# Kernel optimization log

Hardware: AMD Instinct MI355X
Metric: run time of the kernel (lower is better)

## Reference

```python
import jax, jax.numpy as jnp
import numpy as np

N, E, H, OUT, L = 50000, 500000, 256, 128, 2
EPS = 1e-5  # torch LayerNorm default


def _make_edges(k):
    # both rows cover all N nodes so that unique()/remap in the original is identity
    k1, k2, kp = jax.random.split(k, 3)
    row0 = jnp.concatenate([jax.random.permutation(kp, N), jax.random.randint(k1, (E - N,), 0, N)])
    row1 = jnp.concatenate([jnp.arange(N), jax.random.randint(k2, (E - N,), 0, N)])
    return jnp.stack([row0, row1]).astype(jnp.int32)


def setup_inputs() -> dict:
    key = jax.random.key(0)
    ks = jax.random.split(key, 7)
    s = 0.02
    x = jax.random.normal(ks[0], (N, H), jnp.float32)
    edge_r1 = _make_edges(ks[1])
    edge_r2 = _make_edges(ks[2])
    Wl = jax.random.normal(ks[3], (L, H, H), jnp.float32) * s
    W0 = jax.random.normal(ks[4], (L, H, H), jnp.float32) * s
    W1 = jax.random.normal(ks[5], (L, H, H), jnp.float32) * s
    bl = jnp.zeros((L, H), jnp.float32)
    b0 = jnp.zeros((L, H), jnp.float32)
    b1 = jnp.zeros((L, H), jnp.float32)
    gamma = jnp.ones((L, H), jnp.float32)
    beta = jnp.zeros((L, H), jnp.float32)
    Wout = jax.random.normal(ks[6], (OUT, H), jnp.float32) * s
    bout = jnp.zeros((OUT,), jnp.float32)
    return dict(x=x, edge_r1=edge_r1, edge_r2=edge_r2, Wl=Wl, bl=bl, W0=W0, b0=b0,
                W1=W1, b1=b1, gamma=gamma, beta=beta, Wout=Wout, bout=bout)


def _layer(i, h, x0, e, Wl, bl, W0, b0, W1, b1, gamma, beta):
    # PyG flow='target_to_source', aggr='add': gather h at e[1], scatter-add at e[0]
    agg = jax.ops.segment_sum(h[e[1]], e[0], num_segments=h.shape[0])  # [N, H]
    z = agg @ Wl[i].T + bl[i] + h @ W0[i].T + b0[i] + x0 @ W1[i].T + b1[i]
    z = jax.nn.relu(z)
    mu = jnp.mean(z, axis=-1, keepdims=True)
    var = jnp.mean(jnp.square(z - mu), axis=-1, keepdims=True)
    return (z - mu) * jax.lax.rsqrt(var + EPS) * gamma[i] + beta[i]  # dropout is identity in eval


def reference(x, edge_r1, edge_r2, Wl, bl, W0, b0, W1, b1, gamma, beta, Wout, bout):
    # reversed(metapath): (C,r2,C) with conv_idx=1 first, then (C,r1,C) with conv_idx=0
    h = _layer(1, x, x, edge_r2, Wl, bl, W0, b0, W1, b1, gamma, beta)
    h = _layer(0, h, x, edge_r1, Wl, bl, W0, b0, W1, b1, gamma, beta)
    return h @ Wout.T + bout  # [N, OUT]
```

## Files before the change

kernel.cpp:

```cpp
#include <hip/hip_runtime.h>
#include <stdint.h>

#define N_NODES 50000
#define N_EDGES 500000
#define NPAD    50048
#define NSCAN   196
#define EPS     1e-5f

typedef _Float16 half8_ __attribute__((ext_vector_type(8)));
typedef _Float16 half4_ __attribute__((ext_vector_type(4)));
typedef float    float4_ __attribute__((ext_vector_type(4)));

typedef uint32_t u32_g __attribute__((address_space(1)));
typedef uint32_t u32_s __attribute__((address_space(3)));

__device__ __forceinline__ void gload16(const void* g, void* lds_wave_base) {
    __builtin_amdgcn_global_load_lds((const u32_g*)g, (u32_s*)lds_wave_base, 16, 0, 0);
}

__global__ __launch_bounds__(256) void prep_kernel(
        const int* __restrict__ e1, const int* __restrict__ e2,
        int* __restrict__ cnt, int* __restrict__ ranks,
        const float* __restrict__ x, _Float16* __restrict__ xh,
        _Float16* __restrict__ aggb, _Float16* __restrict__ h1,
        const float* __restrict__ Wl, const float* __restrict__ W0,
        const float* __restrict__ W1, const float* __restrict__ Wout,
        _Float16* __restrict__ Wcat,
        const float* __restrict__ bl, const float* __restrict__ b0,
        const float* __restrict__ b1, const float* __restrict__ bout,
        float* __restrict__ bias) {
    const int bid = blockIdx.x;
    const int tid = threadIdx.x;
    if (bid < 490) {
        const int set = (bid >= 245);
        const int bx  = set ? bid - 245 : bid;
        const int* dst = set ? e2 : e1;
        int* c = cnt + set * N_NODES;
        int* r = ranks + set * N_EDGES;
        int i0 = (bx * 256 + tid) * 8;
        if (i0 >= N_EDGES) return;
        int4 d0 = *(const int4*)(dst + i0);
        int4 d1 = *(const int4*)(dst + i0 + 4);
        int r0 = atomicAdd(&c[d0.x], 1);
        int r1 = atomicAdd(&c[d0.y], 1);
        int r2 = atomicAdd(&c[d0.z], 1);
        int r3 = atomicAdd(&c[d0.w], 1);
        int r4 = atomicAdd(&c[d1.x], 1);
        int r5 = atomicAdd(&c[d1.y], 1);
        int r6 = atomicAdd(&c[d1.z], 1);
        int r7 = atomicAdd(&c[d1.w], 1);
        *(int4*)(r + i0)     = make_int4(r0, r1, r2, r3);
        *(int4*)(r + i0 + 4) = make_int4(r4, r5, r6, r7);
    } else if (bid < 12990) {
        int i = (bid - 490) * 256 + tid;
        float4_ v = ((const float4_*)x)[i];
        half4_ h;
        h[0] = (_Float16)v[0]; h[1] = (_Float16)v[1];
        h[2] = (_Float16)v[2]; h[3] = (_Float16)v[3];
        ((half4_*)xh)[i] = h;
    } else if (bid < 14654) {
        int i = (bid - 12990) * 256 + tid;
        if (i < 2 * 256 * 768) {
            int l = i / (256 * 768);
            int r = i % (256 * 768);
            int j = r / 768, k = r % 768;
            const float* s = (k < 256) ? Wl : (k < 512 ? W0 : W1);
            Wcat[i] = (_Float16)s[l * 65536 + j * 256 + (k & 255)];
        } else {
            Wcat[i] = (_Float16)Wout[i - 2 * 256 * 768];
        }
    } else if (bid < 14690) {
        int j = (bid - 14654) * 256 + tid;
        int buf = j / 3072, jj = j % 3072;
        _Float16* p = (buf == 0) ? xh : (buf == 1) ? aggb : h1;
        half4_ z = {(_Float16)0.f, (_Float16)0.f, (_Float16)0.f, (_Float16)0.f};
        *(half4_*)(p + (size_t)N_NODES * 256 + (size_t)jj * 4) = z;
    } else {
        int i = (bid - 14690) * 256 + tid;
        if (i < 512)      bias[i] = bl[i] + b0[i] + b1[i];
        else if (i < 640) bias[i] = bout[i - 512];
    }
}

__global__ __launch_bounds__(256) void scan_kernel(const int* __restrict__ cnt,
                                                   unsigned long long* __restrict__ state,
                                                   int* __restrict__ rp) {
    __shared__ int sm[256];
    __shared__ int s_excl;
    const int bid = blockIdx.x;
    const int set = bid / NSCAN;
    const int seq = bid % NSCAN;
    const int t = threadIdx.x;
    const int i = seq * 256 + t;
    const int* c = cnt + set * N_NODES;
    int* rpS = rp + set * (N_NODES + 1);
    unsigned long long* st = state + set * NSCAN;

    int v = (i < N_NODES) ? c[i] : 0;
    sm[t] = v;
    __syncthreads();
    for (int off = 1; off < 256; off <<= 1) {
        int x = sm[t];
        if (t >= off) x += sm[t - off];
        __syncthreads();
        sm[t] = x;
        __syncthreads();
    }
    int total = sm[255];

    if (t == 0) {
        if (seq == 0) {
            atomicExch(&st[0], (2ULL << 32) | (unsigned int)total);
            s_excl = 0;
        } else {
            atomicExch(&st[seq], (1ULL << 32) | (unsigned int)total);
            int running = 0;
            int j = seq - 1;
            while (true) {
                unsigned long long s = atomicAdd(&st[j], 0ULL);
                unsigned int tag = (unsigned int)(s >> 32);
                if (tag == 0) continue;
                running += (int)(unsigned int)s;
                if (tag == 2) break;
                j--;
            }
            atomicExch(&st[seq], (2ULL << 32) | (unsigned int)(running + total));
            s_excl = running;
        }
    }
    __syncthreads();
    int excl = s_excl;
    if (i < N_NODES) rpS[i] = sm[t] - v + excl;
    if (seq == NSCAN - 1 && t == 0) rpS[N_NODES] = excl + total;
}

__global__ void place_kernel(const int* __restrict__ e1, const int* __restrict__ e2,
                             const int* __restrict__ ranks, const int* __restrict__ rp,
                             int* __restrict__ col, int e, int n) {
    const int set = blockIdx.y;
    const int* ed = set ? e2 : e1;
    const int* r  = ranks + set * e;
    const int* rpS = rp + set * (n + 1);
    int* cl = col + set * e;
    int i0 = (blockIdx.x * 256 + threadIdx.x) * 8;
    if (i0 >= e) return;
    int4 d0 = *(const int4*)(ed + i0);
    int4 d1 = *(const int4*)(ed + i0 + 4);
    int4 s0 = *(const int4*)(ed + e + i0);
    int4 s1 = *(const int4*)(ed + e + i0 + 4);
    int4 k0 = *(const int4*)(r + i0);
    int4 k1 = *(const int4*)(r + i0 + 4);
    int p0 = rpS[d0.x] + k0.x;
    int p1 = rpS[d0.y] + k0.y;
    int p2 = rpS[d0.z] + k0.z;
    int p3 = rpS[d0.w] + k0.w;
    int p4 = rpS[d1.x] + k1.x;
    int p5 = rpS[d1.y] + k1.y;
    int p6 = rpS[d1.z] + k1.z;
    int p7 = rpS[d1.w] + k1.w;
    cl[p0] = s0.x; cl[p1] = s0.y; cl[p2] = s0.z; cl[p3] = s0.w;
    cl[p4] = s1.x; cl[p5] = s1.y; cl[p6] = s1.z; cl[p7] = s1.w;
}

__global__ void gather_kernel(const _Float16* __restrict__ hin,
                              const int* __restrict__ rowptr, const int* __restrict__ col,
                              _Float16* __restrict__ dst, int n) {
    int node = blockIdx.x * 4 + (threadIdx.x >> 6);
    int lane = threadIdx.x & 63;
    int half = lane >> 5, l5 = lane & 31;
    if (node >= n) return;
    int s = rowptr[node], e = rowptr[node + 1];
    float a[8] = {0.f, 0.f, 0.f, 0.f, 0.f, 0.f, 0.f, 0.f};
    float b[8] = {0.f, 0.f, 0.f, 0.f, 0.f, 0.f, 0.f, 0.f};
    int i = s + half;
    for (; i + 2 < e; i += 4) {
        int c0 = col[i], c1 = col[i + 2];
        half8_ v0 = *(const half8_*)(hin + (size_t)c0 * 256 + l5 * 8);
        half8_ v1 = *(const half8_*)(hin + (size_t)c1 * 256 + l5 * 8);
#pragma unroll
        for (int j = 0; j < 8; j++) { a[j] += (float)v0[j]; b[j] += (float)v1[j]; }
    }
    for (; i < e; i += 2) {
        int c0 = col[i];
        half8_ v0 = *(const half8_*)(hin + (size_t)c0 * 256 + l5 * 8);
#pragma unroll
        for (int j = 0; j < 8; j++) a[j] += (float)v0[j];
    }
    half8_ o;
#pragma unroll
    for (int j = 0; j < 8; j++) {
        float t = a[j] + b[j];
        t += __shfl_xor(t, 32, 64);
        o[j] = (_Float16)t;
    }
    if (half == 0)
        *(half8_*)(dst + (size_t)node * 256 + l5 * 8) = o;
}

template <bool OUTFUSE>
__global__ __launch_bounds__(512) void gemm_ln(const _Float16* __restrict__ agg,
                                               const _Float16* __restrict__ hsrc,
                                               const _Float16* __restrict__ xh,
                                               const _Float16* __restrict__ Bw,
                                               const float* __restrict__ bias,
                                               const float* __restrict__ gamma,
                                               const float* __restrict__ beta,
                                               _Float16* __restrict__ H,
                                               const _Float16* __restrict__ WoutH,
                                               const float* __restrict__ biasOut,
                                               float* __restrict__ Out) {
    __shared__ __align__(16) char smem[49152];
    char* AsB = smem;
    char* BsB = smem + 16384;
    const int rowBase = blockIdx.x * 128;
    const int tid  = threadIdx.x;
    const int lane = tid & 63;
    const int w    = tid >> 6;
    const int wm = w & 1, wn = w >> 1;
    const int quad = lane >> 4, mr = lane & 15;
    const int x7 = mr & 7;

    float4_ acc[4][4];
#pragma unroll
    for (int i = 0; i < 4; i++)
#pragma unroll
        for (int j = 0; j < 4; j++) { float4_ z4 = {0.f, 0.f, 0.f, 0.f}; acc[i][j] = z4; }

    int cA0 = w * 64 + lane, cA1 = cA0 + 512;
    int rA0 = cA0 >> 3, rA1 = cA1 >> 3;
    size_t offA0 = (size_t)(rowBase + rA0) * 256 + (((cA0 & 7) ^ (rA0 & 7)) * 8);
    size_t offA1 = (size_t)(rowBase + rA1) * 256 + (((cA1 & 7) ^ (rA1 & 7)) * 8);
    size_t offB[4];
#pragma unroll
    for (int j = 0; j < 4; j++) {
        int c = j * 512 + w * 64 + lane;
        int r = c >> 3;
        offB[j] = (size_t)r * 768 + (((c & 7) ^ (r & 7)) * 8);
    }
    void* lA0 = AsB + w * 1024;
    void* lA1 = AsB + 8192 + w * 1024;

    for (int k0 = 0; k0 < 768; k0 += 64) {
        const _Float16* src = (k0 < 256) ? agg : (k0 < 512) ? hsrc : xh;
        const int kloc = k0 & 255;
        gload16(src + offA0 + kloc, lA0);
        gload16(src + offA1 + kloc, lA1);
        gload16(Bw + offB[0] + k0, BsB + w * 1024);
        gload16(Bw + offB[1] + k0, BsB + 8192 + w * 1024);
        gload16(Bw + offB[2] + k0, BsB + 16384 + w * 1024);
        gload16(Bw + offB[3] + k0, BsB + 24576 + w * 1024);
        __syncthreads();
#pragma unroll
        for (int s = 0; s < 2; s++) {
            half8_ a[4], b[4];
#pragma unroll
            for (int im = 0; im < 4; im++) {
                int row = wm * 64 + im * 16 + mr;
                a[im] = *(const half8_*)(AsB + row * 128 + (((s * 4 + quad) ^ x7) * 16));
            }
#pragma unroll
            for (int in = 0; in < 4; in++) {
                int row = wn * 64 + in * 16 + mr;
                b[in] = *(const half8_*)(BsB + row * 128 + (((s * 4 + quad) ^ x7) * 16));
            }
#pragma unroll
            for (int im = 0; im < 4; im++)
#pragma unroll
                for (int in = 0; in < 4; in++)
                    acc[im][in] = __builtin_amdgcn_mfma_f32_16x16x32_f16(a[im], b[in], acc[im][in], 0, 0, 0);
        }
        __syncthreads();
    }

    float bv[4], gv[4], bev[4];
#pragma unroll
    for (int in = 0; in < 4; in++) {
        int colg = wn * 64 + in * 16 + mr;
        bv[in]  = bias[colg];
        gv[in]  = gamma[colg];
        bev[in] = beta[colg];
    }
    float* lnbuf   = (float*)AsB;
    float* lnstats = (float*)(AsB + 4096);

#pragma unroll
    for (int im = 0; im < 4; im++)
#pragma unroll
        for (int r = 0; r < 4; r++) {
            float s = 0.f, sq = 0.f;
#pragma unroll
            for (int in = 0; in < 4; in++) {
                float v = acc[im][in][r] + bv[in];
                v = v > 0.f ? v : 0.f;
                s += v; sq += v * v;
            }
            s  += __shfl_xor(s, 1, 64);  sq += __shfl_xor(sq, 1, 64);
            s  += __shfl_xor(s, 2, 64);  sq += __shfl_xor(sq, 2, 64);
            s  += __shfl_xor(s, 4, 64);  sq += __shfl_xor(sq, 4, 64);
            s  += __shfl_xor(s, 8, 64);  sq += __shfl_xor(sq, 8, 64);
            if (mr == 0) {
                int rl = wm * 64 + im * 16 + quad * 4 + r;
                lnbuf[(wn * 128 + rl) * 2]     = s;
                lnbuf[(wn * 128 + rl) * 2 + 1] = sq;
            }
        }
    __syncthreads();
    if (tid < 128) {
        float s  = lnbuf[tid * 2]             + lnbuf[(128 + tid) * 2]
                 + lnbuf[(256 + tid) * 2]     + lnbuf[(384 + tid) * 2];
        float sq = lnbuf[tid * 2 + 1]         + lnbuf[(128 + tid) * 2 + 1]
                 + lnbuf[(256 + tid) * 2 + 1] + lnbuf[(384 + tid) * 2 + 1];
        float mu  = s * (1.0f / 256.0f);
        float var = sq * (1.0f / 256.0f) - mu * mu;
        lnstats[tid * 2]     = mu;
        lnstats[tid * 2 + 1] = rsqrtf(var + EPS);
    }
    __syncthreads();

    float bvo[4];
    if (OUTFUSE) {
#pragma unroll
        for (int ct = 0; ct < 4; ct++)
            bvo[ct] = biasOut[(w >> 2) * 64 + ct * 16 + mr];
    }

    _Float16* BsH = (_Float16*)BsB;
#pragma unroll
    for (int p = 0; p < 2; p++) {
        if (wm == p) {
#pragma unroll
            for (int im = 0; im < 4; im++)
#pragma unroll
                for (int r = 0; r < 4; r++) {
                    int rl = im * 16 + quad * 4 + r;
                    float mu = lnstats[(p * 64 + rl) * 2];
                    float rs = lnstats[(p * 64 + rl) * 2 + 1];
#pragma unroll
                    for (int in = 0; in < 4; in++) {
                        float v = acc[im][in][r] + bv[in];
                        v = v > 0.f ? v : 0.f;
                        int colg = wn * 64 + in * 16 + mr;
                        int off2 = rl * 256 + (((colg >> 3) ^ (rl & 31)) << 3) + (colg & 7);
                        BsH[off2] = (_Float16)((v - mu) * rs * gv[in] + bev[in]);
                    }
                }
        }
        __syncthreads();
        if (!OUTFUSE) {
#pragma unroll
            for (int i = 0; i < 4; i++) {
                int c = i * 512 + tid;
                int row = c >> 5, ch = c & 31;
                half8_ v = *(const half8_*)(BsB + row * 512 + ((ch ^ (row & 31)) << 4));
                *(half8_*)(H + (size_t)(rowBase + p * 64 + row) * 256 + ch * 8) = v;
            }
        } else {
            const int rt = w & 3;
            const int chh = w >> 2;
            float4_ acc2[4];
#pragma unroll
            for (int ct = 0; ct < 4; ct++) { float4_ z4 = {0.f, 0.f, 0.f, 0.f}; acc2[ct] = z4; }
            const int rA = rt * 16 + mr;
#pragma unroll
            for (int s2 = 0; s2 < 8; s2++) {
                int ck = s2 * 4 + quad;
                half8_ a2 = *(const half8_*)(BsB + rA * 512 + ((ck ^ (rA & 31)) << 4));
#pragma unroll
                for (int ct = 0; ct < 4; ct++) {
                    int colg = chh * 64 + ct * 16 + mr;
                    half8_ b2 = *(const half8_*)(WoutH + (size_t)colg * 256 + s2 * 32 + quad * 8);
                    acc2[ct] = __builtin_amdgcn_mfma_f32_16x16x32_f16(a2, b2, acc2[ct], 0, 0, 0);
                }
            }
#pragma unroll
            for (int ct = 0; ct < 4; ct++) {
                int colg = chh * 64 + ct * 16 + mr;
#pragma unroll
                for (int r = 0; r < 4; r++) {
                    int row = rowBase + p * 64 + rt * 16 + quad * 4 + r;
                    if (row < N_NODES)
                        Out[(size_t)row * 128 + colg] = acc2[ct][r] + bvo[ct];
                }
            }
        }
        __syncthreads();
    }
}

extern "C" void kernel_launch(void* const* d_in, const int* in_sizes, int n_in,
                              void* d_out, int out_size, void* d_ws, size_t ws_size,
                              hipStream_t stream) {
    const float* x    = (const float*)d_in[0];
    const int*   e1   = (const int*)d_in[1];
    const int*   e2   = (const int*)d_in[2];
    const float* Wl   = (const float*)d_in[3];
    const float* bl   = (const float*)d_in[4];
    const float* W0   = (const float*)d_in[5];
    const float* b0   = (const float*)d_in[6];
    const float* W1   = (const float*)d_in[7];
    const float* b1   = (const float*)d_in[8];
    const float* gamma= (const float*)d_in[9];
    const float* beta = (const float*)d_in[10];
    const float* Wout = (const float*)d_in[11];
    const float* bout = (const float*)d_in[12];

    char* ws = (char*)d_ws;
    size_t off = 0;
    auto alloc = [&](size_t bytes) -> char* {
        char* p = ws + off;
        off = (off + bytes + 255) & ~(size_t)255;
        return p;
    };
    _Float16* xh   = (_Float16*)alloc((size_t)NPAD * 256 * 2);
    _Float16* aggb = (_Float16*)alloc((size_t)NPAD * 256 * 2);
    _Float16* h1   = (_Float16*)alloc((size_t)NPAD * 256 * 2);
    _Float16* Wcat = (_Float16*)alloc((size_t)(2 * 256 * 768 + 128 * 256) * 2);
    float*    bias = (float*)alloc(640 * 4);
    int* cnt   = (int*)alloc((size_t)2 * N_NODES * 4);
    unsigned long long* states = (unsigned long long*)alloc((size_t)2 * NSCAN * 8);
    int* rp    = (int*)alloc((size_t)2 * (N_NODES + 1) * 4);
    int* ranks = (int*)alloc((size_t)2 * N_EDGES * 4);
    int* col   = (int*)alloc((size_t)2 * N_EDGES * 4);

    int* rp1 = rp, *rp2 = rp + (N_NODES + 1);
    int* col1 = col, *col2 = col + N_EDGES;

    size_t zbytes = (size_t)((char*)states + 2 * NSCAN * 8 - (char*)cnt);
    hipMemsetAsync(cnt, 0, zbytes, stream);

    prep_kernel<<<14693, 256, 0, stream>>>(e1, e2, cnt, ranks, x, xh, aggb, h1,
                                           Wl, W0, W1, Wout, Wcat,
                                           bl, b0, b1, bout, bias);
    scan_kernel<<<2 * NSCAN, 256, 0, stream>>>(cnt, states, rp);
    const int eb8 = (N_EDGES / 8 + 255) / 256;
    place_kernel<<<dim3(eb8, 2), 256, 0, stream>>>(e1, e2, ranks, rp, col, N_EDGES, N_NODES);

    const int nb4 = (N_NODES + 3) / 4;
    const _Float16* WoutH = Wcat + 393216;

    gather_kernel<<<nb4, 256, 0, stream>>>(xh, rp2, col2, aggb, N_NODES);
    gemm_ln<false><<<391, 512, 0, stream>>>(aggb, xh, xh, Wcat + 196608,
                                            bias + 256, gamma + 256, beta + 256, h1,
                                            nullptr, nullptr, nullptr);
    gather_kernel<<<nb4, 256, 0, stream>>>(h1, rp1, col1, aggb, N_NODES);
    gemm_ln<true><<<391, 512, 0, stream>>>(aggb, h1, xh, Wcat,
                                           bias, gamma, beta, nullptr,
                                           WoutH, bias + 512, (float*)d_out);
}
```

Before: 370.9 us.

## Unfuse output projection into separate GEMM and widen gather unroll

The final output projection is moved out of the second GEMM+LayerNorm kernel into a separate tiled MFMA GEMM kernel, which reads the normalized hidden state from a new fp16 buffer. The LDS staging in gemm_ln drops the XOR swizzle and uses a plain row layout. The gather loop is unrolled to four neighbor loads per half-wave iteration to put more memory requests in flight. The unfusion adds a global write and read of the hidden state plus an extra launch, and the unswizzled LDS layout may cause bank conflicts.

```diff
diff --git a/kernel.cpp b/kernel.cpp
--- a/kernel.cpp
+++ b/kernel.cpp
@@ -173,12 +173,17 @@
     float a[8] = {0.f, 0.f, 0.f, 0.f, 0.f, 0.f, 0.f, 0.f};
     float b[8] = {0.f, 0.f, 0.f, 0.f, 0.f, 0.f, 0.f, 0.f};
     int i = s + half;
-    for (; i + 2 < e; i += 4) {
-        int c0 = col[i], c1 = col[i + 2];
+    for (; i + 6 < e; i += 8) {
+        int c0 = col[i], c1 = col[i + 2], c2 = col[i + 4], c3 = col[i + 6];
         half8_ v0 = *(const half8_*)(hin + (size_t)c0 * 256 + l5 * 8);
         half8_ v1 = *(const half8_*)(hin + (size_t)c1 * 256 + l5 * 8);
-#pragma unroll
-        for (int j = 0; j < 8; j++) { a[j] += (float)v0[j]; b[j] += (float)v1[j]; }
+        half8_ v2 = *(const half8_*)(hin + (size_t)c2 * 256 + l5 * 8);
+        half8_ v3 = *(const half8_*)(hin + (size_t)c3 * 256 + l5 * 8);
+#pragma unroll
+        for (int j = 0; j < 8; j++) {
+            a[j] += (float)v0[j] + (float)v2[j];
+            b[j] += (float)v1[j] + (float)v3[j];
+        }
     }
     for (; i < e; i += 2) {
         int c0 = col[i];
@@ -197,7 +202,6 @@
         *(half8_*)(dst + (size_t)node * 256 + l5 * 8) = o;
 }
 
-template <bool OUTFUSE>
 __global__ __launch_bounds__(512) void gemm_ln(const _Float16* __restrict__ agg,
                                                const _Float16* __restrict__ hsrc,
                                                const _Float16* __restrict__ xh,
@@ -205,10 +209,7 @@
                                                const float* __restrict__ bias,
                                                const float* __restrict__ gamma,
                                                const float* __restrict__ beta,
-                                               _Float16* __restrict__ H,
-                                               const _Float16* __restrict__ WoutH,
-                                               const float* __restrict__ biasOut,
-                                               float* __restrict__ Out) {
+                                               _Float16* __restrict__ H) {
     __shared__ __align__(16) char smem[49152];
     char* AsB = smem;
     char* BsB = smem + 16384;
@@ -317,13 +318,6 @@
     }
     __syncthreads();
 
-    float bvo[4];
-    if (OUTFUSE) {
-#pragma unroll
-        for (int ct = 0; ct < 4; ct++)
-            bvo[ct] = biasOut[(w >> 2) * 64 + ct * 16 + mr];
-    }
-
     _Float16* BsH = (_Float16*)BsB;
 #pragma unroll
     for (int p = 0; p < 2; p++) {
@@ -339,51 +333,92 @@
                     for (int in = 0; in < 4; in++) {
                         float v = acc[im][in][r] + bv[in];
                         v = v > 0.f ? v : 0.f;
-                        int colg = wn * 64 + in * 16 + mr;
-                        int off2 = rl * 256 + (((colg >> 3) ^ (rl & 31)) << 3) + (colg & 7);
-                        BsH[off2] = (_Float16)((v - mu) * rs * gv[in] + bev[in]);
+                        BsH[rl * 256 + wn * 64 + in * 16 + mr] =
+                            (_Float16)((v - mu) * rs * gv[in] + bev[in]);
                     }
                 }
         }
         __syncthreads();
-        if (!OUTFUSE) {
-#pragma unroll
-            for (int i = 0; i < 4; i++) {
-                int c = i * 512 + tid;
-                int row = c >> 5, ch = c & 31;
-                half8_ v = *(const half8_*)(BsB + row * 512 + ((ch ^ (row & 31)) << 4));
-                *(half8_*)(H + (size_t)(rowBase + p * 64 + row) * 256 + ch * 8) = v;
-            }
-        } else {
-            const int rt = w & 3;
-            const int chh = w >> 2;
-            float4_ acc2[4];
-#pragma unroll
-            for (int ct = 0; ct < 4; ct++) { float4_ z4 = {0.f, 0.f, 0.f, 0.f}; acc2[ct] = z4; }
-            const int rA = rt * 16 + mr;
-#pragma unroll
-            for (int s2 = 0; s2 < 8; s2++) {
-                int ck = s2 * 4 + quad;
-                half8_ a2 = *(const half8_*)(BsB + rA * 512 + ((ck ^ (rA & 31)) << 4));
-#pragma unroll
-                for (int ct = 0; ct < 4; ct++) {
-                    int colg = chh * 64 + ct * 16 + mr;
-                    half8_ b2 = *(const half8_*)(WoutH + (size_t)colg * 256 + s2 * 32 + quad * 8);
-                    acc2[ct] = __builtin_amdgcn_mfma_f32_16x16x32_f16(a2, b2, acc2[ct], 0, 0, 0);
-                }
-            }
-#pragma unroll
-            for (int ct = 0; ct < 4; ct++) {
-                int colg = chh * 64 + ct * 16 + mr;
-#pragma unroll
-                for (int r = 0; r < 4; r++) {
-                    int row = rowBase + p * 64 + rt * 16 + quad * 4 + r;
-                    if (row < N_NODES)
-                        Out[(size_t)row * 128 + colg] = acc2[ct][r] + bvo[ct];
-                }
-            }
-        }
-        __syncthreads();
+#pragma unroll
+        for (int i = 0; i < 4; i++) {
+            int c = i * 512 + tid;
+            int row = c >> 5, ch = c & 31;
+            half8_ v = *(const half8_*)(BsB + c * 16);
+            *(half8_*)(H + (size_t)(rowBase + p * 64 + row) * 256 + ch * 8) = v;
+        }
+        __syncthreads();
+    }
+}
+
+__global__ __launch_bounds__(256) void gemm_bt(const _Float16* __restrict__ A, int lda,
+                                               const _Float16* __restrict__ B, int ldb,
+                                               const float* __restrict__ bias,
+                                               float* __restrict__ C, int ldc,
+                                               int K, int Mstore) {
+    __shared__ _Float16 As[128 * 32];
+    __shared__ _Float16 Bs[128 * 32];
+    const int rowBase = blockIdx.x * 128;
+    const int colBase = blockIdx.y * 128;
+    const int tid  = threadIdx.x;
+    const int lane = tid & 63;
+    const int w    = tid >> 6;
+    const int wm = w & 1, wn = w >> 1;
+    const int quad = lane >> 4, mr = lane & 15;
+
+    float4_ acc[4][4];
+#pragma unroll
+    for (int i = 0; i < 4; i++)
+#pragma unroll
+        for (int j = 0; j < 4; j++) { float4_ z4 = {0.f, 0.f, 0.f, 0.f}; acc[i][j] = z4; }
+
+    const int c0  = w * 64 + lane;
+    const int rA0 = c0 >> 2;
+    const int ko  = (c0 & 3) * 8;
+    char* AsB = (char*)As;
+    char* BsB = (char*)Bs;
+    void* lA0 = AsB + w * 1024;
+    void* lA1 = AsB + 4096 + w * 1024;
+    void* lB0 = BsB + w * 1024;
+    void* lB1 = BsB + 4096 + w * 1024;
+    const _Float16* gA0 = A + (size_t)(rowBase + rA0) * lda + ko;
+    const _Float16* gA1 = gA0 + (size_t)64 * lda;
+    const _Float16* gB0 = B + (size_t)(colBase + rA0) * ldb + ko;
+    const _Float16* gB1 = gB0 + (size_t)64 * ldb;
+
+    for (int k0 = 0; k0 < K; k0 += 32) {
+        gload16(gA0 + k0, lA0);
+        gload16(gA1 + k0, lA1);
+        gload16(gB0 + k0, lB0);
+        gload16(gB1 + k0, lB1);
+        __syncthreads();
+        half8_ a[4], b[4];
+#pragma unroll
+        for (int im = 0; im < 4; im++)
+            a[im] = *(const half8_*)(AsB + ((wm * 64 + im * 16 + mr) * 64 + quad * 16));
+#pragma unroll
+        for (int in = 0; in < 4; in++)
+            b[in] = *(const half8_*)(BsB + ((wn * 64 + in * 16 + mr) * 64 + quad * 16));
+#pragma unroll
+        for (int im = 0; im < 4; im++)
+#pragma unroll
+            for (int in = 0; in < 4; in++)
+                acc[im][in] = __builtin_amdgcn_mfma_f32_16x16x32_f16(a[im], b[in], acc[im][in], 0, 0, 0);
+        __syncthreads();
+    }
+
+#pragma unroll
+    for (int in = 0; in < 4; in++) {
+        const int colg = colBase + wn * 64 + in * 16 + mr;
+        const float bv = bias[colg];
+#pragma unroll
+        for (int im = 0; im < 4; im++) {
+            float4_ c = acc[im][in];
+#pragma unroll
+            for (int r = 0; r < 4; r++) {
+                int row = rowBase + wm * 64 + im * 16 + quad * 4 + r;
+                if (row < Mstore) C[(size_t)row * ldc + colg] = c[r] + bv;
+            }
+        }
     }
 }
 
@@ -414,6 +449,7 @@
     _Float16* xh   = (_Float16*)alloc((size_t)NPAD * 256 * 2);
     _Float16* aggb = (_Float16*)alloc((size_t)NPAD * 256 * 2);
     _Float16* h1   = (_Float16*)alloc((size_t)NPAD * 256 * 2);
+    _Float16* h2   = (_Float16*)alloc((size_t)NPAD * 256 * 2);
     _Float16* Wcat = (_Float16*)alloc((size_t)(2 * 256 * 768 + 128 * 256) * 2);
     float*    bias = (float*)alloc(640 * 4);
     int* cnt   = (int*)alloc((size_t)2 * N_NODES * 4);
@@ -439,11 +475,11 @@
     const _Float16* WoutH = Wcat + 393216;
 
     gather_kernel<<<nb4, 256, 0, stream>>>(xh, rp2, col2, aggb, N_NODES);
-    gemm_ln<false><<<391, 512, 0, stream>>>(aggb, xh, xh, Wcat + 196608,
-                                            bias + 256, gamma + 256, beta + 256, h1,
-                                            nullptr, nullptr, nullptr);
+    gemm_ln<<<391, 512, 0, stream>>>(aggb, xh, xh, Wcat + 196608,
+                                     bias + 256, gamma + 256, beta + 256, h1);
     gather_kernel<<<nb4, 256, 0, stream>>>(h1, rp1, col1, aggb, N_NODES);
-    gemm_ln<true><<<391, 512, 0, stream>>>(aggb, h1, xh, Wcat,
-                                           bias, gamma, beta, nullptr,
-                                           WoutH, bias + 512, (float*)d_out);
-}
+    gemm_ln<<<391, 512, 0, stream>>>(aggb, h1, xh, Wcat,
+                                     bias, gamma, beta, h2);
+    gemm_bt<<<dim3(391, 1), 256, 0, stream>>>(h2, 256, WoutH, 256,
+                                              bias + 512, (float*)d_out, 128, 256, N_NODES);
+}
```

Result: faster. 345.4 us (-6.9%).
